# Performance work log

Measured on AMD Instinct MI355X. Metric: run time of the kernel, lower is better.

Reference implementation:

```python
import jax, jax.numpy as jnp
import numpy as np

N, L, D, H = 2, 2048, 2048, 16
HD = D // H  # head_dim = 128


def setup_inputs() -> dict:
    key = jax.random.key(0)
    k1, k2, k3, k4 = jax.random.split(key, 4)
    x = jax.random.normal(k1, (N, L, D), dtype=jnp.float32)
    pos = jax.random.normal(k2, (2, L, HD), dtype=jnp.float32)
    w_qkv = jax.random.normal(k3, (3 * D, D), dtype=jnp.float32) * (D ** -0.5)
    w_o = jax.random.normal(k4, (D, D), dtype=jnp.float32) * (D ** -0.5)
    return {"x": x, "pos": pos, "w_qkv": w_qkv, "w_o": w_o}


def rotate_half(t):
    t1, t2 = jnp.split(t, 2, axis=-1)
    return jnp.concatenate((-t2, t1), axis=-1)


def reference(x, pos, w_qkv, w_o):
    n, l, d = x.shape
    h, hd = H, HD
    qkv = jnp.einsum('nld,ed->nle', x, w_qkv)  # [N,L,3D]
    q, k, v = jnp.split(qkv, 3, axis=-1)
    q = q.reshape(n, l, h, hd)
    k = k.reshape(n, l, h, hd)
    v = v.reshape(n, l, h, hd)
    cos = pos[0][None, :, None, :]  # [1,L,1,HD]
    sin = pos[1][None, :, None, :]
    q = q * cos + rotate_half(q) * sin
    k = k * cos + rotate_half(k) * sin
    scale = hd ** -0.5
    scores = jnp.einsum('nlhd,nmhd->nhlm', q, k) * scale  # [N,H,L,L]
    causal = jnp.tril(jnp.ones((l, l), dtype=bool))
    scores = jnp.where(causal[None, None], scores, jnp.finfo(scores.dtype).min)
    attn = jax.nn.softmax(scores, axis=-1)
    o = jnp.einsum('nhlm,nmhd->nlhd', attn, v).reshape(n, l, d)
    return jnp.einsum('nld,ed->nle', o, w_o)
```

## Files before the change

### kernel.cpp

```cpp
#include <hip/hip_runtime.h>

typedef __attribute__((ext_vector_type(8))) short short8;
typedef __attribute__((ext_vector_type(4))) float f32x4;

#define NB 2
#define SEQ 2048
#define DM 2048
#define NHEAD 16
#define HDIM 128

__device__ __forceinline__ unsigned short f2bf(float f) {
    unsigned u = __float_as_uint(f);
    u += 0x7fffu + ((u >> 16) & 1u);
    return (unsigned short)(u >> 16);
}
__device__ __forceinline__ float bf2f(unsigned short h) {
    return __uint_as_float(((unsigned)h) << 16);
}
__device__ __forceinline__ unsigned pk2bf(float a, float b) {
    return (unsigned)f2bf(a) | ((unsigned)f2bf(b) << 16);
}
__device__ __forceinline__ void gload16(const unsigned short* g, unsigned short* l) {
    __builtin_amdgcn_global_load_lds((const __attribute__((address_space(1))) void*)g,
                                     (__attribute__((address_space(3))) void*)l,
                                     16, 0, 0);
}

__global__ __launch_bounds__(256) void cvt_bf16(const float* __restrict__ a,
                                                unsigned short* __restrict__ oa, int na8,
                                                const float* __restrict__ b,
                                                unsigned short* __restrict__ ob, int nb8)
{
    const int t0 = blockIdx.x * 256 + threadIdx.x;
    const int stride = gridDim.x * 256;
    for (int i = t0; i < na8; i += stride) {
        const f32x4* src = (const f32x4*)(a + (size_t)i * 8);
        f32x4 lo = src[0], hi = src[1];
        short8 v;
#pragma unroll
        for (int j = 0; j < 4; ++j) { v[j] = (short)f2bf(lo[j]); v[j + 4] = (short)f2bf(hi[j]); }
        *(short8*)(oa + (size_t)i * 8) = v;
    }
    for (int i = t0; i < nb8; i += stride) {
        const f32x4* src = (const f32x4*)(b + (size_t)i * 8);
        f32x4 lo = src[0], hi = src[1];
        short8 v;
#pragma unroll
        for (int j = 0; j < 4; ++j) { v[j] = (short)f2bf(lo[j]); v[j + 4] = (short)f2bf(hi[j]); }
        *(short8*)(ob + (size_t)i * 8) = v;
    }
}

template<int EPI, int CPX>
__global__ __launch_bounds__(256) void gemm_m97(const unsigned short* __restrict__ A,
                                                const unsigned short* __restrict__ B,
                                                int K,
                                                unsigned short* __restrict__ qb,
                                                unsigned short* __restrict__ kb,
                                                unsigned short* __restrict__ vtb,
                                                const float* __restrict__ posp,
                                                float* __restrict__ outf)
{
    __shared__ unsigned short smem[16384];
    const int tid = threadIdx.x;
    const int lane = tid & 63, w = tid >> 6;
    const int wr = w >> 1, wc = w & 1;
    const int g = lane >> 4, fr = lane & 15;
    const int lr = lane >> 2, ls = lane & 3;
    const int x = blockIdx.x & 7, t = blockIdx.x >> 3;
    const int rp = t / (2 * CPX), wi = t % (2 * CPX);
    const int bx = x * CPX + (wi % CPX), by = rp * 2 + wi / CPX;
    const int row0 = by * 128, col0 = bx * 128;

    auto stage = [&](int b, int kt) {
        const int k0 = kt * 32;
#pragma unroll
        for (int c = 0; c < 2; ++c) {
            const int r = c * 64 + w * 16;
            gload16(A + (size_t)(row0 + r + lr) * K + k0 + ls * 8,
                    smem + b * 4096 + r * 32);
            gload16(B + (size_t)(col0 + r + lr) * K + k0 + ls * 8,
                    smem + 8192 + b * 4096 + r * 32);
        }
    };

    const f32x4 fz = {0.f, 0.f, 0.f, 0.f};
    f32x4 acc[4][4];
#pragma unroll
    for (int m = 0; m < 4; ++m)
#pragma unroll
        for (int n = 0; n < 4; ++n) acc[m][n] = fz;

    const int nk = K / 32;
    stage(0, 0);
    __syncthreads();
    for (int kt = 0; kt < nk; ++kt) {
        const int cur = kt & 1;
        if (kt + 1 < nk) stage(cur ^ 1, kt + 1);
        short8 af[4], bfv[4];
#pragma unroll
        for (int m = 0; m < 4; ++m)
            af[m] = *(const short8*)&smem[cur * 4096 + (wr * 64 + m * 16 + fr) * 32 + g * 8];
#pragma unroll
        for (int n = 0; n < 4; ++n)
            bfv[n] = *(const short8*)&smem[8192 + cur * 4096 + (wc * 64 + n * 16 + fr) * 32 + g * 8];
#pragma unroll
        for (int m = 0; m < 4; ++m)
#pragma unroll
            for (int n = 0; n < 4; ++n)
                acc[m][n] = __builtin_amdgcn_mfma_f32_16x16x32_bf16(
                    af[m], bfv[n], acc[m][n], 0, 0, 0);
        __syncthreads();
    }

    if constexpr (EPI == 0) {
#pragma unroll
        for (int m = 0; m < 4; ++m)
#pragma unroll
            for (int n = 0; n < 4; ++n)
#pragma unroll
                for (int r = 0; r < 4; ++r) {
                    int rr = row0 + wr * 64 + m * 16 + g * 4 + r;
                    int cc = col0 + wc * 64 + n * 16 + fr;
                    outf[(size_t)rr * 2048 + cc] = acc[m][n][r];
                }
    } else {
        const int which = col0 >> 11;
        const int hB = (col0 >> 7) & 15;
        if (which < 2) {
#pragma unroll
            for (int m = 0; m < 4; ++m)
#pragma unroll
                for (int n = 0; n < 4; ++n)
#pragma unroll
                    for (int r = 0; r < 4; ++r) {
                        int rl = wr * 64 + m * 16 + g * 4 + r;
                        int cl = wc * 64 + n * 16 + fr;
                        smem[rl * 128 + cl] = f2bf(acc[m][n][r]);
                    }
            __syncthreads();
            unsigned short* dst = which ? kb : qb;
#pragma unroll
            for (int m = 0; m < 4; ++m)
#pragma unroll
                for (int n = 0; n < 4; ++n)
#pragma unroll
                    for (int r = 0; r < 4; ++r) {
                        int rl = wr * 64 + m * 16 + g * 4 + r;
                        int cl = wc * 64 + n * 16 + fr;
                        int rr = row0 + rl;
                        int l = rr & 2047, nb_ = rr >> 11;
                        float own = acc[m][n][r];
                        float pr = bf2f(smem[rl * 128 + (cl ^ 64)]);
                        float c = posp[(size_t)l * HDIM + cl];
                        float s = posp[(size_t)SEQ * HDIM + (size_t)l * HDIM + cl];
                        float res = (cl < 64) ? (own * c - pr * s) : (own * c + pr * s);
                        size_t hb = (size_t)(nb_ * NHEAD + hB) * ((size_t)SEQ * HDIM);
                        dst[hb + (size_t)l * HDIM + cl] = f2bf(res);
                    }
        } else {
#pragma unroll
            for (int m = 0; m < 4; ++m)
#pragma unroll
                for (int n = 0; n < 4; ++n)
#pragma unroll
                    for (int r = 0; r < 4; ++r) {
                        int rr = row0 + wr * 64 + m * 16 + g * 4 + r;
                        int cl = wc * 64 + n * 16 + fr;
                        int l = rr & 2047, nb_ = rr >> 11;
                        size_t hb = (size_t)(nb_ * NHEAD + hB) * ((size_t)SEQ * HDIM);
                        vtb[hb + (size_t)cl * SEQ + l] = f2bf(acc[m][n][r]);
                    }
        }
    }
}

__global__ __launch_bounds__(256, 2) void attn_k(const unsigned short* __restrict__ Q,
                                                 const unsigned short* __restrict__ K,
                                                 const unsigned short* __restrict__ VT,
                                                 unsigned short* __restrict__ O)
{
    const int lb = blockIdx.x;
    const int xcd = lb & 7, idx = lb >> 3;
    const int nh = xcd * 4 + (idx >> 4);
    const int p = idx & 15;
    const int tid = threadIdx.x;
    const int w = tid >> 6, lane = tid & 63;
    const int g = lane >> 4, fr = lane & 15;
    const float scale = 0.08838834764831845f;

    const unsigned short* Qh = Q + (size_t)nh * SEQ * HDIM;
    const unsigned short* Kh = K + (size_t)nh * SEQ * HDIM;
    const unsigned short* Vh = VT + (size_t)nh * SEQ * HDIM;
    const int nb = nh >> 4, h = nh & 15;

    __shared__ unsigned short Kt[2][8192];
    __shared__ unsigned short Vt[2][8192];
    __shared__ unsigned Plds[4][576];

    auto stage = [&](int bf, int kbi) {
        const int key0 = kbi * 64;
#pragma unroll
        for (int c = 0; c < 4; ++c) {
            int r = c * 16 + (tid >> 4);
            int sK = tid & 15;
            gload16(Kh + (size_t)(key0 + r) * HDIM + 8 * (sK ^ (r & 7)),
                    &Kt[bf][c * 2048 + w * 512]);
            int d = c * 32 + (tid >> 3);
            int sV = tid & 7;
            gload16(Vh + (size_t)d * SEQ + key0 + 8 * (sV ^ (d & 7)),
                    &Vt[bf][c * 2048 + w * 512]);
        }
    };

    for (int pass = 0; pass < 2; ++pass) {
        const int tile = pass ? (15 - p) : p;
        const int qt = tile * 128 + w * 32;
        const int nkb_w = (qt + 31) >> 6;
        const int nkb_blk = 2 * tile + 1;

        short8 qf[2][4];
#pragma unroll
        for (int u = 0; u < 2; ++u)
#pragma unroll
            for (int kk = 0; kk < 4; ++kk)
                qf[u][kk] = *(const short8*)(Qh + (size_t)(qt + u * 16 + fr) * HDIM + kk * 32 + g * 8);

        const f32x4 fz = {0.f, 0.f, 0.f, 0.f};
        f32x4 oacc[2][8];
#pragma unroll
        for (int u = 0; u < 2; ++u)
#pragma unroll
            for (int f = 0; f < 8; ++f) oacc[u][f] = fz;
        float mrow[2] = {-3e38f, -3e38f}, lrow[2] = {0.f, 0.f};

        stage(0, 0);
        int buf = 0;
        __syncthreads();

        for (int kbi = 0; kbi <= nkb_blk; ++kbi) {
            if (kbi < nkb_blk) stage(buf ^ 1, kbi + 1);

            if (kbi <= nkb_w) {
                const int key0 = kbi * 64;
                f32x4 s[2][4];
#pragma unroll
                for (int u = 0; u < 2; ++u)
#pragma unroll
                    for (int hh = 0; hh < 4; ++hh) s[u][hh] = fz;

                __builtin_amdgcn_s_setprio(1);
#pragma unroll
                for (int hh = 0; hh < 4; ++hh) {
                    short8 kfh[4];
#pragma unroll
                    for (int kk = 0; kk < 4; ++kk)
                        kfh[kk] = *(const short8*)&Kt[buf][(hh * 16 + fr) * 128 + 8 * ((4 * kk + g) ^ (fr & 7))];
#pragma unroll
                    for (int u = 0; u < 2; ++u)
#pragma unroll
                        for (int kk = 0; kk < 4; ++kk)
                            s[u][hh] = __builtin_amdgcn_mfma_f32_16x16x32_bf16(kfh[kk], qf[u][kk], s[u][hh], 0, 0, 0);
                }
                __builtin_amdgcn_s_setprio(0);

#pragma unroll
                for (int u = 0; u < 2; ++u) {
                    const int q = qt + u * 16 + fr;
#pragma unroll
                    for (int hh = 0; hh < 4; ++hh)
#pragma unroll
                        for (int r = 0; r < 4; ++r) {
                            int key = key0 + hh * 16 + 4 * g + r;
                            float v = s[u][hh][r] * scale;
                            s[u][hh][r] = (key <= q) ? v : -1e30f;
                        }
                    float mx = -3e38f;
#pragma unroll
                    for (int hh = 0; hh < 4; ++hh)
                        mx = fmaxf(mx, fmaxf(fmaxf(s[u][hh][0], s[u][hh][1]),
                                             fmaxf(s[u][hh][2], s[u][hh][3])));
                    mx = fmaxf(mx, __shfl_xor(mx, 16, 64));
                    mx = fmaxf(mx, __shfl_xor(mx, 32, 64));
                    if (!__all(mx <= mrow[u] + 8.f)) {
                        float mn = fmaxf(mrow[u], mx);
                        float al = __expf(mrow[u] - mn);
                        mrow[u] = mn;
                        lrow[u] *= al;
#pragma unroll
                        for (int f = 0; f < 8; ++f)
#pragma unroll
                            for (int r = 0; r < 4; ++r) oacc[u][f][r] *= al;
                    }
                    float pv[4][4];
                    float ps = 0.f;
#pragma unroll
                    for (int hh = 0; hh < 4; ++hh)
#pragma unroll
                        for (int r = 0; r < 4; ++r) {
                            float e = __expf(s[u][hh][r] - mrow[u]);
                            pv[hh][r] = e;
                            ps += e;
                        }
                    ps += __shfl_xor(ps, 16, 64);
                    ps += __shfl_xor(ps, 32, 64);
                    lrow[u] += ps;
                    unsigned* Pw = &Plds[w][0];
#pragma unroll
                    for (int hh = 0; hh < 4; ++hh) {
                        Pw[fr * 36 + hh * 8 + 2 * g + 0] = pk2bf(pv[hh][0], pv[hh][1]);
                        Pw[fr * 36 + hh * 8 + 2 * g + 1] = pk2bf(pv[hh][2], pv[hh][3]);
                    }
                    asm volatile("s_waitcnt lgkmcnt(0)" ::: "memory");
                    short8 pf0 = *(const short8*)&Pw[fr * 36 + g * 4];
                    short8 pf1 = *(const short8*)&Pw[fr * 36 + 16 + g * 4];

                    __builtin_amdgcn_s_setprio(1);
#pragma unroll
                    for (int f = 0; f < 8; ++f) {
                        short8 vfa = *(const short8*)&Vt[buf][(f * 16 + fr) * 64 + 8 * (g ^ (fr & 7))];
                        short8 vfb = *(const short8*)&Vt[buf][(f * 16 + fr) * 64 + 8 * ((4 + g) ^ (fr & 7))];
                        oacc[u][f] = __builtin_amdgcn_mfma_f32_16x16x32_bf16(vfa, pf0, oacc[u][f], 0, 0, 0);
                        oacc[u][f] = __builtin_amdgcn_mfma_f32_16x16x32_bf16(vfb, pf1, oacc[u][f], 0, 0, 0);
                    }
                    __builtin_amdgcn_s_setprio(0);
                }
            }
            __syncthreads();
            buf ^= 1;
        }

#pragma unroll
        for (int u = 0; u < 2; ++u) {
            const float inv = 1.0f / lrow[u];
            const size_t obase = ((size_t)nb * SEQ + qt + u * 16 + fr) * DM + h * HDIM;
#pragma unroll
            for (int f = 0; f < 8; ++f) {
                unsigned w0 = pk2bf(oacc[u][f][0] * inv, oacc[u][f][1] * inv);
                unsigned w1 = pk2bf(oacc[u][f][2] * inv, oacc[u][f][3] * inv);
                unsigned* dstp = (unsigned*)(O + obase + f * 16 + 4 * g);
                dstp[0] = w0;
                dstp[1] = w1;
            }
        }
    }
}

extern "C" void kernel_launch(void* const* d_in, const int* in_sizes, int n_in,
                              void* d_out, int out_size, void* d_ws, size_t ws_size,
                              hipStream_t stream) {
    const float* x    = (const float*)d_in[0];
    const float* pos  = (const float*)d_in[1];
    const float* wqkv = (const float*)d_in[2];
    const float* wo   = (const float*)d_in[3];
    float* out = (float*)d_out;

    const size_t HBUF = (size_t)NB * NHEAD * SEQ * HDIM;
    unsigned short* qb   = (unsigned short*)d_ws;
    unsigned short* kbuf = qb + HBUF;
    unsigned short* vtb  = kbuf + HBUF;
    unsigned short* obx  = vtb + HBUF;
    unsigned short* wqkvbf = (unsigned short*)d_out;

    cvt_bf16<<<dim3(2048), 256, 0, stream>>>(x, obx, 1048576, wqkv, wqkvbf, 1572864);
    gemm_m97<1, 6><<<dim3(1536), 256, 0, stream>>>(obx, wqkvbf, 2048, qb, kbuf, vtb, pos, nullptr);
    attn_k<<<dim3(512), 256, 0, stream>>>(qb, kbuf, vtb, obx);
    cvt_bf16<<<dim3(512), 256, 0, stream>>>(wo, qb, 524288, wo, qb, 0);
    gemm_m97<0, 2><<<dim3(512), 256, 0, stream>>>(obx, qb, 2048, nullptr, nullptr, nullptr, nullptr, out);
}
```

Baseline: 325.7 us.

## Replace QKV GEMM with 256x256-tile 8-wave pipelined kernel

Adds a new QKV projection kernel using 256x256 output tiles, 512 threads, 128KB of swizzled LDS with double buffering, and an 8-phase schedule. The schedule interleaves global-to-LDS staging, LDS fragment loads and MFMA quadrants, using explicit waitcnt, sched_barrier and setprio. The aim is to raise arithmetic intensity, hide memory latency and cut LDS bank conflicts compared with the old 128x128 tile kernel. It also remaps blocks so that groups of column tiles stay on the same XCD. In exchange, register pressure is higher, there are only 384 blocks (limited occupancy or wave tail), and the hand-written phase ordering is fragile.

```diff
diff --git a/kernel.cpp b/kernel.cpp
--- a/kernel.cpp
+++ b/kernel.cpp
@@ -48,6 +48,162 @@
 #pragma unroll
         for (int j = 0; j < 4; ++j) { v[j] = (short)f2bf(lo[j]); v[j + 4] = (short)f2bf(hi[j]); }
         *(short8*)(ob + (size_t)i * 8) = v;
+    }
+}
+
+__global__ __launch_bounds__(512, 2) void gemm8p_qkv(const unsigned short* __restrict__ Ap,
+                                                     const unsigned short* __restrict__ Bp,
+                                                     unsigned short* __restrict__ qb,
+                                                     unsigned short* __restrict__ kb,
+                                                     unsigned short* __restrict__ vtb,
+                                                     const float* __restrict__ posp)
+{
+    __shared__ unsigned char smem[131072];
+    const int tid = threadIdx.x;
+    const int w = tid >> 6, lane = tid & 63;
+    const int wr = w >> 2, wcn = w & 3;
+    const int g = lane >> 4, fr = lane & 15;
+    const int x = blockIdx.x & 7, t = blockIdx.x >> 3;
+    const int bx = x * 3 + t % 3, by = t / 3;
+    const int row0 = by * 256, col0 = bx * 256;
+
+    const int rr_ = lane >> 2, sl_ = lane & 3;
+    const int slotp = sl_ ^ (((rr_ >> 3) & 1) << 1);
+    const int stgCol = (w & 1) * 32 + slotp * 8;
+    const int stgRow0 = (w >> 1) * 16 + rr_;
+    const int stgRow1 = 64 + (w >> 1) * 16 + rr_;
+    const int rdoff = fr * 64 + (g ^ (((fr >> 3) & 1) << 1)) * 16;
+    const int aRdHalf = wr * 16384;
+    const int bRdHalf = 65536 + (wcn >> 1) * 16384;
+    const int bRgBase = (wcn & 1) * 4;
+
+#define STG(o, h, kt, d) do { \
+    gload16(((o) ? Bp : Ap) + (size_t)(((o) ? col0 : row0) + (h) * 128 + stgRow0) * 2048 + (size_t)(kt) * 64 + stgCol, \
+            (unsigned short*)(smem + (o) * 65536 + (d) * 32768 + (h) * 16384 + w * 1024)); \
+    gload16(((o) ? Bp : Ap) + (size_t)(((o) ? col0 : row0) + (h) * 128 + stgRow1) * 2048 + (size_t)(kt) * 64 + stgCol, \
+            (unsigned short*)(smem + (o) * 65536 + (d) * 32768 + (h) * 16384 + 8192 + w * 1024)); \
+} while (0)
+
+#define LOAD_A(BLK, D) do { \
+    _Pragma("unroll") for (int mi = 0; mi < 4; ++mi) \
+    _Pragma("unroll") for (int kk = 0; kk < 2; ++kk) \
+        af[BLK][mi][kk] = *(const short8*)(smem + (D) * 32768 + aRdHalf + (((BLK) * 4 + mi) * 2 + kk) * 1024 + rdoff); \
+} while (0)
+
+#define LOAD_B(BLK, D) do { \
+    _Pragma("unroll") for (int ni = 0; ni < 2; ++ni) \
+    _Pragma("unroll") for (int kk = 0; kk < 2; ++kk) \
+        bf[BLK][ni][kk] = *(const short8*)(smem + (D) * 32768 + bRdHalf + ((bRgBase + (BLK) * 2 + ni) * 2 + kk) * 1024 + rdoff); \
+} while (0)
+
+#define MFMAQ(MQ, NQ) do { \
+    _Pragma("unroll") for (int mi = 0; mi < 4; ++mi) \
+    _Pragma("unroll") for (int ni = 0; ni < 2; ++ni) \
+    _Pragma("unroll") for (int kk = 0; kk < 2; ++kk) \
+        acc[(MQ) * 4 + mi][(NQ) * 2 + ni] = __builtin_amdgcn_mfma_f32_16x16x32_bf16( \
+            af[MQ][mi][kk], bf[NQ][ni][kk], acc[(MQ) * 4 + mi][(NQ) * 2 + ni], 0, 0, 0); \
+} while (0)
+
+#define PHASE(P) do { \
+    if (((P) & 3) == 0) LOAD_A(1, (P) >> 2); \
+    if (((P) & 3) == 1) LOAD_B(1, (P) >> 2); \
+    if (((P) & 3) == 3) { if (!(last && (P) == 7)) { LOAD_A(0, ((P) >> 2) ^ 1); LOAD_B(0, ((P) >> 2) ^ 1); } } \
+    if ((P) == 0) STG(1, 0, 2 * i + 1, 1); \
+    if ((P) == 1) STG(1, 1, 2 * i + 1, 1); \
+    if ((P) == 2 && !last) STG(0, 0, 2 * i + 2, 0); \
+    if ((P) == 3 && !last) STG(0, 1, 2 * i + 2, 0); \
+    if ((P) == 4 && !last) STG(1, 0, 2 * i + 2, 0); \
+    if ((P) == 5 && !last) STG(1, 1, 2 * i + 2, 0); \
+    if ((P) == 6 && !last) STG(0, 0, 2 * i + 3, 1); \
+    if ((P) == 7 && !last) STG(0, 1, 2 * i + 3, 1); \
+    __builtin_amdgcn_s_barrier(); \
+    asm volatile("s_waitcnt lgkmcnt(0)" ::: "memory"); \
+    __builtin_amdgcn_sched_barrier(0); \
+    __builtin_amdgcn_s_setprio(1); \
+    MFMAQ((P) & 1, ((P) >> 1) & 1); \
+    __builtin_amdgcn_s_setprio(0); \
+    if ((P) == 2) { if (last) asm volatile("s_waitcnt vmcnt(0)" ::: "memory"); \
+                    else      asm volatile("s_waitcnt vmcnt(2)" ::: "memory"); \
+                    __builtin_amdgcn_sched_barrier(0); } \
+    if ((P) == 6 && !last) { asm volatile("s_waitcnt vmcnt(2)" ::: "memory"); \
+                             __builtin_amdgcn_sched_barrier(0); } \
+    __builtin_amdgcn_s_barrier(); \
+} while (0)
+
+    const f32x4 fz = {0.f, 0.f, 0.f, 0.f};
+    f32x4 acc[8][4];
+#pragma unroll
+    for (int m = 0; m < 8; ++m)
+#pragma unroll
+        for (int n = 0; n < 4; ++n) acc[m][n] = fz;
+    short8 af[2][4][2], bf[2][2][2];
+
+    STG(0, 0, 0, 0); STG(0, 1, 0, 0); STG(1, 0, 0, 0); STG(1, 1, 0, 0);
+    STG(0, 0, 1, 1); STG(0, 1, 1, 1);
+    asm volatile("s_waitcnt vmcnt(0)" ::: "memory");
+    __syncthreads();
+    LOAD_A(0, 0); LOAD_B(0, 0);
+
+    for (int i = 0; i < 16; ++i) {
+        const bool last = (i == 15);
+        PHASE(0); PHASE(1); PHASE(2); PHASE(3);
+        PHASE(4); PHASE(5); PHASE(6); PHASE(7);
+    }
+#undef PHASE
+#undef MFMAQ
+#undef LOAD_A
+#undef LOAD_B
+#undef STG
+
+    unsigned short* sm16 = (unsigned short*)smem;
+#pragma unroll
+    for (int m = 0; m < 8; ++m)
+#pragma unroll
+        for (int n = 0; n < 4; ++n)
+#pragma unroll
+            for (int r2 = 0; r2 < 4; ++r2) {
+                int rl = wr * 128 + m * 16 + g * 4 + r2;
+                int cl = wcn * 64 + n * 16 + fr;
+                sm16[rl * 256 + cl] = f2bf(acc[m][n][r2]);
+            }
+    __syncthreads();
+    const int which = col0 >> 11;
+    if (which < 2) {
+        unsigned short* dst = which ? kb : qb;
+#pragma unroll
+        for (int m = 0; m < 8; ++m)
+#pragma unroll
+            for (int n = 0; n < 4; ++n)
+#pragma unroll
+                for (int r2 = 0; r2 < 4; ++r2) {
+                    int rl = wr * 128 + m * 16 + g * 4 + r2;
+                    int cl = wcn * 64 + n * 16 + fr;
+                    int rrg = row0 + rl;
+                    int l = rrg & 2047, nb_ = rrg >> 11;
+                    int cc = col0 + cl;
+                    int hB = (cc >> 7) & 15, hd = cc & 127;
+                    float own = acc[m][n][r2];
+                    float pr = bf2f(sm16[rl * 256 + (cl ^ 64)]);
+                    float c = posp[(size_t)l * HDIM + hd];
+                    float s = posp[(size_t)SEQ * HDIM + (size_t)l * HDIM + hd];
+                    float res = (hd < 64) ? (own * c - pr * s) : (own * c + pr * s);
+                    dst[(size_t)(nb_ * NHEAD + hB) * ((size_t)SEQ * HDIM) + (size_t)l * HDIM + hd] = f2bf(res);
+                }
+    } else {
+#pragma unroll
+        for (int m = 0; m < 8; ++m)
+#pragma unroll
+            for (int n = 0; n < 4; ++n)
+#pragma unroll
+                for (int r2 = 0; r2 < 4; ++r2) {
+                    int rl = wr * 128 + m * 16 + g * 4 + r2;
+                    int cl = wcn * 64 + n * 16 + fr;
+                    int rrg = row0 + rl;
+                    int l = rrg & 2047, nb_ = rrg >> 11;
+                    int cc = col0 + cl;
+                    int hB = (cc >> 7) & 15, hd = cc & 127;
+                    vtb[(size_t)(nb_ * NHEAD + hB) * ((size_t)SEQ * HDIM) + (size_t)hd * SEQ + l] = f2bf(acc[m][n][r2]);
+                }
     }
 }
 
@@ -97,10 +253,10 @@
     for (int kt = 0; kt < nk; ++kt) {
         const int cur = kt & 1;
         if (kt + 1 < nk) stage(cur ^ 1, kt + 1);
-        short8 af[4], bfv[4];
+        short8 af2[4], bfv[4];
 #pragma unroll
         for (int m = 0; m < 4; ++m)
-            af[m] = *(const short8*)&smem[cur * 4096 + (wr * 64 + m * 16 + fr) * 32 + g * 8];
+            af2[m] = *(const short8*)&smem[cur * 4096 + (wr * 64 + m * 16 + fr) * 32 + g * 8];
 #pragma unroll
         for (int n = 0; n < 4; ++n)
             bfv[n] = *(const short8*)&smem[8192 + cur * 4096 + (wc * 64 + n * 16 + fr) * 32 + g * 8];
@@ -109,70 +265,20 @@
 #pragma unroll
             for (int n = 0; n < 4; ++n)
                 acc[m][n] = __builtin_amdgcn_mfma_f32_16x16x32_bf16(
-                    af[m], bfv[n], acc[m][n], 0, 0, 0);
+                    af2[m], bfv[n], acc[m][n], 0, 0, 0);
         __syncthreads();
     }
 
-    if constexpr (EPI == 0) {
-#pragma unroll
-        for (int m = 0; m < 4; ++m)
-#pragma unroll
-            for (int n = 0; n < 4; ++n)
-#pragma unroll
-                for (int r = 0; r < 4; ++r) {
-                    int rr = row0 + wr * 64 + m * 16 + g * 4 + r;
-                    int cc = col0 + wc * 64 + n * 16 + fr;
-                    outf[(size_t)rr * 2048 + cc] = acc[m][n][r];
-                }
-    } else {
-        const int which = col0 >> 11;
-        const int hB = (col0 >> 7) & 15;
-        if (which < 2) {
-#pragma unroll
-            for (int m = 0; m < 4; ++m)
-#pragma unroll
-                for (int n = 0; n < 4; ++n)
-#pragma unroll
-                    for (int r = 0; r < 4; ++r) {
-                        int rl = wr * 64 + m * 16 + g * 4 + r;
-                        int cl = wc * 64 + n * 16 + fr;
-                        smem[rl * 128 + cl] = f2bf(acc[m][n][r]);
-                    }
-            __syncthreads();
-            unsigned short* dst = which ? kb : qb;
-#pragma unroll
-            for (int m = 0; m < 4; ++m)
-#pragma unroll
-                for (int n = 0; n < 4; ++n)
-#pragma unroll
-                    for (int r = 0; r < 4; ++r) {
-                        int rl = wr * 64 + m * 16 + g * 4 + r;
-                        int cl = wc * 64 + n * 16 + fr;
-                        int rr = row0 + rl;
-                        int l = rr & 2047, nb_ = rr >> 11;
-                        float own = acc[m][n][r];
-                        float pr = bf2f(smem[rl * 128 + (cl ^ 64)]);
-                        float c = posp[(size_t)l * HDIM + cl];
-                        float s = posp[(size_t)SEQ * HDIM + (size_t)l * HDIM + cl];
-                        float res = (cl < 64) ? (own * c - pr * s) : (own * c + pr * s);
-                        size_t hb = (size_t)(nb_ * NHEAD + hB) * ((size_t)SEQ * HDIM);
-                        dst[hb + (size_t)l * HDIM + cl] = f2bf(res);
-                    }
-        } else {
-#pragma unroll
-            for (int m = 0; m < 4; ++m)
-#pragma unroll
-                for (int n = 0; n < 4; ++n)
-#pragma unroll
-                    for (int r = 0; r < 4; ++r) {
-                        int rr = row0 + wr * 64 + m * 16 + g * 4 + r;
-                        int cl = wc * 64 + n * 16 + fr;
-                        int l = rr & 2047, nb_ = rr >> 11;
-                        size_t hb = (size_t)(nb_ * NHEAD + hB) * ((size_t)SEQ * HDIM);
-                        vtb[hb + (size_t)cl * SEQ + l] = f2bf(acc[m][n][r]);
-                    }
-        }
-    }
+#pragma unroll
+    for (int m = 0; m < 4; ++m)
+#pragma unroll
+        for (int n = 0; n < 4; ++n)
+#pragma unroll
+            for (int r = 0; r < 4; ++r) {
+                int rr = row0 + wr * 64 + m * 16 + g * 4 + r;
+                int cc = col0 + wc * 64 + n * 16 + fr;
+                outf[(size_t)rr * 2048 + cc] = acc[m][n][r];
+            }
 }
 
 __global__ __launch_bounds__(256, 2) void attn_k(const unsigned short* __restrict__ Q,
@@ -363,7 +469,7 @@
     unsigned short* wqkvbf = (unsigned short*)d_out;
 
     cvt_bf16<<<dim3(2048), 256, 0, stream>>>(x, obx, 1048576, wqkv, wqkvbf, 1572864);
-    gemm_m97<1, 6><<<dim3(1536), 256, 0, stream>>>(obx, wqkvbf, 2048, qb, kbuf, vtb, pos, nullptr);
+    gemm8p_qkv<<<dim3(384), 512, 0, stream>>>(obx, wqkvbf, qb, kbuf, vtb, pos);
     attn_k<<<dim3(512), 256, 0, stream>>>(qb, kbuf, vtb, obx);
     cvt_bf16<<<dim3(512), 256, 0, stream>>>(wo, qb, 524288, wo, qb, 0);
     gemm_m97<0, 2><<<dim3(512), 256, 0, stream>>>(obx, qb, 2048, nullptr, nullptr, nullptr, nullptr, out);
```

Result: slower. 383.2 us (+17.6%).
